# Kernel optimization log

Hardware: AMD Instinct MI355X
Metric: run time of the kernel (lower is better)

The kernel has to match this reference:

```python
import jax, jax.numpy as jnp
import numpy as np

NUM_HEADS = 8
ROPE_BASE = 10000.0

def rotate_half(x):
    x1, x2 = jnp.split(x, 2, axis=-1)
    return jnp.concatenate((-x2, x1), axis=-1)

def rope_cos_sin(seq_len, head_dim, dtype):
    inv_freq = 1.0 / (ROPE_BASE ** (jnp.arange(0, head_dim, 2, dtype=jnp.float32) / head_dim))
    t = jnp.arange(seq_len, dtype=jnp.float32)
    freqs = t[:, None] * inv_freq[None, :]            # [N, D/2]
    emb = jnp.concatenate((freqs, freqs), axis=-1)    # [N, D]
    cos = jnp.cos(emb)[None, None].astype(dtype)      # [1,1,N,D]
    sin = jnp.sin(emb)[None, None].astype(dtype)
    return cos, sin

def setup_inputs() -> dict:
    key = jax.random.key(0)
    k1, k2, k3 = jax.random.split(key, 3)
    B, N, C = 4, 2048, 512
    x = jax.random.normal(k1, (B, N, C), dtype=jnp.float32)
    w_qkv = jax.random.normal(k2, (C, 3 * C), dtype=jnp.float32) * (C ** -0.5)
    w_proj = jax.random.normal(k3, (C, C), dtype=jnp.float32) * (C ** -0.5)
    b_proj = jnp.zeros((C,), dtype=jnp.float32)
    return {"x": x, "w_qkv": w_qkv, "w_proj": w_proj, "b_proj": b_proj}

def reference(x, w_qkv, w_proj, b_proj):
    B, N, C = x.shape
    H = NUM_HEADS
    D = C // H
    scale = D ** -0.5
    qkv = (x @ w_qkv).reshape(B, N, 3, H, D).transpose(2, 0, 3, 1, 4)  # [3,B,H,N,D]
    q, k, v = qkv[0], qkv[1], qkv[2]
    cos, sin = rope_cos_sin(N, D, x.dtype)
    q = q * cos + rotate_half(q) * sin
    k = k * cos + rotate_half(k) * sin
    attn = jax.nn.softmax(jnp.einsum('bhnd,bhmd->bhnm', q, k) * scale, axis=-1)  # [B,H,N,N]
    out = jnp.einsum('bhnm,bhmd->bhnd', attn, v)      # [B,H,N,D]
    out = out.transpose(0, 2, 1, 3).reshape(B, N, C)
    out = out @ w_proj + b_proj
    return out, attn
```

## Files before the change

kernel.cpp:

```cpp
#include <hip/hip_runtime.h>
#include <math.h>


#define OFF_K 4194304
#define OFF_V 8388608

typedef float nf4 __attribute__((ext_vector_type(4)));

#define SWZ(row, col) (((((col) >> 2) ^ (((row) >> 2) & 7)) << 2) | ((col) & 3))

__global__ __launch_bounds__(256) void gemm_qkv_kernel(
    const float* __restrict__ x, const float* __restrict__ w,
    float* __restrict__ qb, float* __restrict__ kb, float* __restrict__ vb)
{
    __shared__ float As[8][132];
    __shared__ float Bs[8][132];
    const int tid  = threadIdx.x;
    const int row0 = blockIdx.x * 128;
    const int col0 = blockIdx.y * 128;
    const int tx = tid & 15, ty = tid >> 4;

    float acc[8][8];
    #pragma unroll
    for (int i = 0; i < 8; ++i)
        #pragma unroll
        for (int j = 0; j < 8; ++j) acc[i][j] = 0.0f;

    const int ar  = tid >> 1;
    const int ah  = (tid & 1) * 4;
    const int bkr = tid >> 5;
    const int bc  = (tid & 31) * 4;

    for (int k0 = 0; k0 < 512; k0 += 8) {
        float4 a4 = *(const float4*)(x + (size_t)(row0 + ar) * 512 + k0 + ah);
        float4 b4 = *(const float4*)(w + (size_t)(k0 + bkr) * 1536 + col0 + bc);
        __syncthreads();
        As[ah + 0][ar] = a4.x; As[ah + 1][ar] = a4.y;
        As[ah + 2][ar] = a4.z; As[ah + 3][ar] = a4.w;
        *(float4*)&Bs[bkr][bc] = b4;
        __syncthreads();
        #pragma unroll
        for (int kk = 0; kk < 8; ++kk) {
            float a[8], b[8];
            *(float4*)&a[0] = *(const float4*)&As[kk][ty * 8];
            *(float4*)&a[4] = *(const float4*)&As[kk][ty * 8 + 4];
            *(float4*)&b[0] = *(const float4*)&Bs[kk][tx * 8];
            *(float4*)&b[4] = *(const float4*)&Bs[kk][tx * 8 + 4];
            #pragma unroll
            for (int i = 0; i < 8; ++i)
                #pragma unroll
                for (int j = 0; j < 8; ++j)
                    acc[i][j] = fmaf(a[i], b[j], acc[i][j]);
        }
    }

    #pragma unroll
    for (int i = 0; i < 8; ++i) {
        int r  = row0 + ty * 8 + i;
        int b_ = r >> 11;
        int n  = r & 2047;
        #pragma unroll
        for (int j0 = 0; j0 < 8; j0 += 4) {
            int c     = col0 + tx * 8 + j0;
            int which = c >> 9;
            int h     = (c >> 6) & 7;
            int d     = c & 63;
            float* base = (which == 0) ? qb : ((which == 1) ? kb : vb);
            float* dst  = base + (((size_t)(b_ * 8 + h) * 2048 + n) * 64 + d);
            *(float4*)dst = make_float4(acc[i][j0], acc[i][j0 + 1],
                                        acc[i][j0 + 2], acc[i][j0 + 3]);
        }
    }
}

__global__ void rope_table_kernel(float2* __restrict__ tab)
{
    int idx = blockIdx.x * 256 + threadIdx.x;
    if (idx >= 2048 * 32) return;
    int i = idx & 31;
    int n = idx >> 5;
    double invf = pow(10000.0, -(double)(2 * i) / 64.0);
    double ang  = (double)n * invf;
    tab[idx] = make_float2((float)cos(ang), (float)sin(ang));
}

__global__ void rope_apply_kernel(float* __restrict__ qb, float* __restrict__ kb,
                                  const float2* __restrict__ tab)
{
    int idx = blockIdx.x * 256 + threadIdx.x;
    if (idx >= 4 * 8 * 2048 * 32) return;
    int i  = idx & 31;
    int n  = (idx >> 5) & 2047;
    int bh = idx >> 16;

    float2 cs = tab[(n << 5) | i];
    float c = cs.x, s = cs.y;

    size_t base = ((size_t)bh * 2048 + n) * 64;
    float q0 = qb[base + i], q1 = qb[base + i + 32];
    qb[base + i]      = q0 * c - q1 * s;
    qb[base + i + 32] = q1 * c + q0 * s;
    float k0 = kb[base + i], k1 = kb[base + i + 32];
    kb[base + i]      = k0 * c - k1 * s;
    kb[base + i + 32] = k1 * c + k0 * s;
}

__global__ __launch_bounds__(256) void attn_scores_pv_kernel(
    const float* __restrict__ qb, const float* __restrict__ kb,
    const float* __restrict__ vb, float* __restrict__ attn,
    float* __restrict__ out_pre)
{
    __shared__ float smem[18560];
    float (*Qs)[128] = (float (*)[128])smem;
    float (*Ks)[128] = (float (*)[128])(smem + 8192);
    float (*Ps)[128] = (float (*)[128])smem;
    float (*Vs)[68]  = (float (*)[68])(smem + 8192);
    float (*mt)[16]  = (float (*)[16])(smem + 16384);
    float* l_lds     = smem + 18432;

    const int tid = threadIdx.x;
    const int bh  = blockIdx.x;
    const int n0  = blockIdx.y * 128;
    const int tx = tid & 15, ty = tid >> 4;

    const float* qbase = qb + ((size_t)bh * 2048 + n0) * 64;
    const float* kbase = kb + (size_t)bh * 2048 * 64;
    const float* vbase = vb + (size_t)bh * 2048 * 64;
    float* attn_base = attn + ((size_t)bh * 2048 + n0) * 2048;

    #pragma unroll
    for (int it = 0; it < 8; ++it) {
        int r = ty + it * 16;
        int d = tx * 4;
        float4 v4 = *(const float4*)(qbase + (size_t)r * 64 + d);
        int pc = SWZ(d, r);
        Qs[d + 0][pc] = v4.x * 0.125f; Qs[d + 1][pc] = v4.y * 0.125f;
        Qs[d + 2][pc] = v4.z * 0.125f; Qs[d + 3][pc] = v4.w * 0.125f;
    }
    float m[8], l[8];
    #pragma unroll
    for (int i = 0; i < 8; ++i) { m[i] = -3.0e38f; l[i] = 0.0f; }
    __syncthreads();

    for (int m0 = 0; m0 < 2048; m0 += 128) {
        float4 kv[8];
        #pragma unroll
        for (int it = 0; it < 8; ++it) {
            int c = ty + it * 16;
            kv[it] = *(const float4*)(kbase + (size_t)(m0 + c) * 64 + tx * 4);
        }
        __syncthreads();
        #pragma unroll
        for (int it = 0; it < 8; ++it) {
            int c = ty + it * 16;
            int d = tx * 4;
            int pc = SWZ(d, c);
            Ks[d + 0][pc] = kv[it].x; Ks[d + 1][pc] = kv[it].y;
            Ks[d + 2][pc] = kv[it].z; Ks[d + 3][pc] = kv[it].w;
        }
        __syncthreads();

        float acc[8][8];
        #pragma unroll
        for (int i = 0; i < 8; ++i)
            #pragma unroll
            for (int j = 0; j < 8; ++j) acc[i][j] = 0.0f;

        #pragma unroll 4
        for (int d = 0; d < 64; ++d) {
            const int sk = (d >> 2) & 7;
            float a[8], b[8];
            *(float4*)&a[0] = *(const float4*)&Qs[d][((ty * 2 + 0) ^ sk) << 2];
            *(float4*)&a[4] = *(const float4*)&Qs[d][((ty * 2 + 1) ^ sk) << 2];
            *(float4*)&b[0] = *(const float4*)&Ks[d][((tx * 2 + 0) ^ sk) << 2];
            *(float4*)&b[4] = *(const float4*)&Ks[d][((tx * 2 + 1) ^ sk) << 2];
            #pragma unroll
            for (int i = 0; i < 8; ++i)
                #pragma unroll
                for (int j = 0; j < 8; ++j)
                    acc[i][j] = fmaf(a[i], b[j], acc[i][j]);
        }

        #pragma unroll
        for (int i = 0; i < 8; ++i) {
            float mx = acc[i][0];
            #pragma unroll
            for (int j = 1; j < 8; ++j) mx = fmaxf(mx, acc[i][j]);
            mx = fmaxf(mx, __shfl_xor(mx, 1));
            mx = fmaxf(mx, __shfl_xor(mx, 2));
            mx = fmaxf(mx, __shfl_xor(mx, 4));
            mx = fmaxf(mx, __shfl_xor(mx, 8));
            float mn = fmaxf(m[i], mx);
            l[i] *= __expf(m[i] - mn);
            m[i]  = mn;
            float s = 0.0f;
            #pragma unroll
            for (int j = 0; j < 8; ++j) {
                acc[i][j] = __expf(acc[i][j] - mn);
                s += acc[i][j];
            }
            s += __shfl_xor(s, 1);
            s += __shfl_xor(s, 2);
            s += __shfl_xor(s, 4);
            s += __shfl_xor(s, 8);
            l[i] += s;
        }

        #pragma unroll
        for (int i = 0; i < 8; ++i) {
            int r = ty * 8 + i;
            float* drow = attn_base + (size_t)r * 2048 + m0 + tx * 8;
            *(float4*)drow       = make_float4(acc[i][0], acc[i][1], acc[i][2], acc[i][3]);
            *(float4*)(drow + 4) = make_float4(acc[i][4], acc[i][5], acc[i][6], acc[i][7]);
        }
        if (tx == 0) {
            int t = m0 >> 7;
            #pragma unroll
            for (int i = 0; i < 8; ++i) mt[ty * 8 + i][t] = m[i];
        }
    }
    if (tx == 0) {
        #pragma unroll
        for (int i = 0; i < 8; ++i) l_lds[ty * 8 + i] = l[i];
    }
    __syncthreads();

    {
        int r  = tid >> 1;
        int c0 = (tid & 1) * 8;
        float v[8];
        #pragma unroll
        for (int j = 0; j < 8; ++j) v[j] = mt[r][c0 + j];
        float mf = mt[r][15];
        float lv = l_lds[r];
        __syncthreads();
        #pragma unroll
        for (int j = 0; j < 8; ++j) mt[r][c0 + j] = __expf(v[j] - mf) / lv;
    }
    __syncthreads();

    float accO[8][4];
    #pragma unroll
    for (int i = 0; i < 8; ++i)
        #pragma unroll
        for (int j = 0; j < 4; ++j) accO[i][j] = 0.0f;

    for (int s0 = 0; s0 < 2048; s0 += 64) {
        const int t = s0 >> 7;
        float4 vv[4];
        #pragma unroll
        for (int it = 0; it < 4; ++it)
            vv[it] = *(const float4*)(vbase + (size_t)(s0 + ty + it * 16) * 64 + tx * 4);

        float4 pp[8];
        #pragma unroll
        for (int it = 0; it < 8; ++it) {
            int r = ty + it * 16;
            float c = mt[r][t];
            float* prow = attn_base + (size_t)r * 2048 + s0 + tx * 4;
            float4 s4 = *(const float4*)prow;
            s4.x *= c; s4.y *= c; s4.z *= c; s4.w *= c;
            pp[it] = s4;
            nf4 nt = { s4.x, s4.y, s4.z, s4.w };
            __builtin_nontemporal_store(nt, (nf4*)prow);
        }

        __syncthreads();
        #pragma unroll
        for (int it = 0; it < 4; ++it)
            *(float4*)&Vs[ty + it * 16][tx * 4] = vv[it];
        #pragma unroll
        for (int it = 0; it < 8; ++it) {
            int r = ty + it * 16;
            int mcol = tx * 4;
            int pc = SWZ(mcol, r);
            Ps[mcol + 0][pc] = pp[it].x; Ps[mcol + 1][pc] = pp[it].y;
            Ps[mcol + 2][pc] = pp[it].z; Ps[mcol + 3][pc] = pp[it].w;
        }
        __syncthreads();

        #pragma unroll 4
        for (int kk = 0; kk < 64; ++kk) {
            const int sk = (kk >> 2) & 7;
            float a[8], b[4];
            *(float4*)&a[0] = *(const float4*)&Ps[kk][((ty * 2 + 0) ^ sk) << 2];
            *(float4*)&a[4] = *(const float4*)&Ps[kk][((ty * 2 + 1) ^ sk) << 2];
            *(float4*)&b[0] = *(const float4*)&Vs[kk][tx * 4];
            #pragma unroll
            for (int i = 0; i < 8; ++i)
                #pragma unroll
                for (int j = 0; j < 4; ++j)
                    accO[i][j] = fmaf(a[i], b[j], accO[i][j]);
        }
    }

    #pragma unroll
    for (int i = 0; i < 8; ++i) {
        float* dst = out_pre + ((size_t)bh * 2048 + n0 + ty * 8 + i) * 64 + tx * 4;
        *(float4*)dst = make_float4(accO[i][0], accO[i][1], accO[i][2], accO[i][3]);
    }
}

__global__ __launch_bounds__(256) void proj_kernel(
    const float* __restrict__ a, const float* __restrict__ w,
    const float* __restrict__ bias, float* __restrict__ out)
{
    __shared__ float As[8][68];
    __shared__ float Bs[8][132];
    const int tid  = threadIdx.x;
    const int row0 = blockIdx.x * 64;
    const int col0 = blockIdx.y * 128;
    const int tx = tid & 31, ty = tid >> 5;

    float acc[8][4];
    #pragma unroll
    for (int i = 0; i < 8; ++i)
        #pragma unroll
        for (int j = 0; j < 4; ++j) acc[i][j] = 0.0f;

    const int ar  = tid >> 1;
    const int ah  = (tid & 1) * 4;
    const int bkr = tid >> 5;
    const int bc  = (tid & 31) * 4;

    const int r_  = row0 + ar;
    const int b_  = r_ >> 11;
    const int n_  = r_ & 2047;

    for (int k0 = 0; k0 < 512; k0 += 8) {
        float4 a4;
        if (tid < 128) {
            const int kk_ = k0 + ah;
            const int h_  = kk_ >> 6;
            const int d_  = kk_ & 63;
            a4 = *(const float4*)(a + (((size_t)(b_ * 8 + h_) * 2048 + n_) * 64 + d_));
        }
        float4 b4 = *(const float4*)(w + (size_t)(k0 + bkr) * 512 + col0 + bc);
        __syncthreads();
        if (tid < 128) {
            As[ah + 0][ar] = a4.x; As[ah + 1][ar] = a4.y;
            As[ah + 2][ar] = a4.z; As[ah + 3][ar] = a4.w;
        }
        *(float4*)&Bs[bkr][bc] = b4;
        __syncthreads();
        #pragma unroll
        for (int kk = 0; kk < 8; ++kk) {
            float av[8], bv[4];
            *(float4*)&av[0] = *(const float4*)&As[kk][ty * 8];
            *(float4*)&av[4] = *(const float4*)&As[kk][ty * 8 + 4];
            *(float4*)&bv[0] = *(const float4*)&Bs[kk][tx * 4];
            #pragma unroll
            for (int i = 0; i < 8; ++i)
                #pragma unroll
                for (int j = 0; j < 4; ++j)
                    acc[i][j] = fmaf(av[i], bv[j], acc[i][j]);
        }
    }

    float bj[4];
    #pragma unroll
    for (int j = 0; j < 4; ++j) bj[j] = bias[col0 + tx * 4 + j];

    #pragma unroll
    for (int i = 0; i < 8; ++i) {
        int r = row0 + ty * 8 + i;
        float* dst = out + (size_t)r * 512 + col0 + tx * 4;
        *(float4*)dst = make_float4(acc[i][0] + bj[0], acc[i][1] + bj[1],
                                    acc[i][2] + bj[2], acc[i][3] + bj[3]);
    }
}

extern "C" void kernel_launch(void* const* d_in, const int* in_sizes, int n_in,
                              void* d_out, int out_size, void* d_ws, size_t ws_size,
                              hipStream_t stream)
{
    const float* x      = (const float*)d_in[0];
    const float* w_qkv  = (const float*)d_in[1];
    const float* w_proj = (const float*)d_in[2];
    const float* b_proj = (const float*)d_in[3];

    float* out  = (float*)d_out;
    float* attn = (float*)d_out + 4194304;

    float* ws = (float*)d_ws;
    float* q = ws;
    float* k = ws + OFF_K;
    float* v = ws + OFF_V;
    float* out_pre = ws;

    float2* rope_tab = (float2*)attn;

    gemm_qkv_kernel<<<dim3(64, 12), 256, 0, stream>>>(x, w_qkv, q, k, v);
    rope_table_kernel<<<256, 256, 0, stream>>>(rope_tab);
    rope_apply_kernel<<<8192, 256, 0, stream>>>(q, k, rope_tab);
    attn_scores_pv_kernel<<<dim3(32, 16), 256, 0, stream>>>(q, k, v, attn, out_pre);
    proj_kernel<<<dim3(128, 4), 256, 0, stream>>>(out_pre, w_proj, b_proj, out);
}
```

Measured before the change: 1.312 ms.

## Fuse RoPE table into apply kernel, pad attention LDS, enlarge proj tiles

Merges the RoPE table generation and application into a single kernel that computes cos/sin once per (n,i) and loops over all batch-head pairs, removing a launch and the table round trip. Pads the attention kernel's shared-memory row stride from 128 to 132 to reduce bank conflicts. Retiles the output projection GEMM to 128x128 blocks with an 8x8 per-thread tile for more register reuse. Risks include lower parallelism in the RoPE kernel, higher register pressure in proj, and the padding interacting with the existing swizzle.

```diff
diff --git a/kernel.cpp b/kernel.cpp
--- a/kernel.cpp
+++ b/kernel.cpp
@@ -73,36 +73,30 @@
     }
 }
 
-__global__ void rope_table_kernel(float2* __restrict__ tab)
+__global__ __launch_bounds__(256) void rope_kernel(
+    float* __restrict__ qb, float* __restrict__ kb)
 {
     int idx = blockIdx.x * 256 + threadIdx.x;
     if (idx >= 2048 * 32) return;
     int i = idx & 31;
     int n = idx >> 5;
+
     double invf = pow(10000.0, -(double)(2 * i) / 64.0);
     double ang  = (double)n * invf;
-    tab[idx] = make_float2((float)cos(ang), (float)sin(ang));
-}
-
-__global__ void rope_apply_kernel(float* __restrict__ qb, float* __restrict__ kb,
-                                  const float2* __restrict__ tab)
-{
-    int idx = blockIdx.x * 256 + threadIdx.x;
-    if (idx >= 4 * 8 * 2048 * 32) return;
-    int i  = idx & 31;
-    int n  = (idx >> 5) & 2047;
-    int bh = idx >> 16;
-
-    float2 cs = tab[(n << 5) | i];
-    float c = cs.x, s = cs.y;
-
-    size_t base = ((size_t)bh * 2048 + n) * 64;
-    float q0 = qb[base + i], q1 = qb[base + i + 32];
-    qb[base + i]      = q0 * c - q1 * s;
-    qb[base + i + 32] = q1 * c + q0 * s;
-    float k0 = kb[base + i], k1 = kb[base + i + 32];
-    kb[base + i]      = k0 * c - k1 * s;
-    kb[base + i + 32] = k1 * c + k0 * s;
+    float c = (float)cos(ang);
+    float s = (float)sin(ang);
+
+    size_t off = (size_t)n * 64 + i;
+    #pragma unroll 4
+    for (int bh = 0; bh < 32; ++bh) {
+        size_t base = (size_t)bh * (2048 * 64) + off;
+        float q0 = qb[base], q1 = qb[base + 32];
+        qb[base]      = q0 * c - q1 * s;
+        qb[base + 32] = q1 * c + q0 * s;
+        float k0 = kb[base], k1 = kb[base + 32];
+        kb[base]      = k0 * c - k1 * s;
+        kb[base + 32] = k1 * c + k0 * s;
+    }
 }
 
 __global__ __launch_bounds__(256) void attn_scores_pv_kernel(
@@ -110,13 +104,13 @@
     const float* __restrict__ vb, float* __restrict__ attn,
     float* __restrict__ out_pre)
 {
-    __shared__ float smem[18560];
-    float (*Qs)[128] = (float (*)[128])smem;
-    float (*Ks)[128] = (float (*)[128])(smem + 8192);
-    float (*Ps)[128] = (float (*)[128])smem;
-    float (*Vs)[68]  = (float (*)[68])(smem + 8192);
-    float (*mt)[16]  = (float (*)[16])(smem + 16384);
-    float* l_lds     = smem + 18432;
+    __shared__ float smem[19072];
+    float (*Qs)[132] = (float (*)[132])smem;
+    float (*Ks)[132] = (float (*)[132])(smem + 8448);
+    float (*Ps)[132] = (float (*)[132])smem;
+    float (*Vs)[68]  = (float (*)[68])(smem + 8448);
+    float (*mt)[16]  = (float (*)[16])(smem + 16896);
+    float* l_lds     = smem + 18944;
 
     const int tid = threadIdx.x;
     const int bh  = blockIdx.x;
@@ -305,18 +299,18 @@
     const float* __restrict__ a, const float* __restrict__ w,
     const float* __restrict__ bias, float* __restrict__ out)
 {
-    __shared__ float As[8][68];
+    __shared__ float As[8][132];
     __shared__ float Bs[8][132];
     const int tid  = threadIdx.x;
-    const int row0 = blockIdx.x * 64;
+    const int row0 = blockIdx.x * 128;
     const int col0 = blockIdx.y * 128;
-    const int tx = tid & 31, ty = tid >> 5;
-
-    float acc[8][4];
+    const int tx = tid & 15, ty = tid >> 4;
+
+    float acc[8][8];
     #pragma unroll
     for (int i = 0; i < 8; ++i)
         #pragma unroll
-        for (int j = 0; j < 4; ++j) acc[i][j] = 0.0f;
+        for (int j = 0; j < 8; ++j) acc[i][j] = 0.0f;
 
     const int ar  = tid >> 1;
     const int ah  = (tid & 1) * 4;
@@ -328,45 +322,43 @@
     const int n_  = r_ & 2047;
 
     for (int k0 = 0; k0 < 512; k0 += 8) {
-        float4 a4;
-        if (tid < 128) {
-            const int kk_ = k0 + ah;
-            const int h_  = kk_ >> 6;
-            const int d_  = kk_ & 63;
-            a4 = *(const float4*)(a + (((size_t)(b_ * 8 + h_) * 2048 + n_) * 64 + d_));
-        }
+        const int kk_ = k0 + ah;
+        const int h_  = kk_ >> 6;
+        const int d_  = kk_ & 63;
+        float4 a4 = *(const float4*)(a + (((size_t)(b_ * 8 + h_) * 2048 + n_) * 64 + d_));
         float4 b4 = *(const float4*)(w + (size_t)(k0 + bkr) * 512 + col0 + bc);
         __syncthreads();
-        if (tid < 128) {
-            As[ah + 0][ar] = a4.x; As[ah + 1][ar] = a4.y;
-            As[ah + 2][ar] = a4.z; As[ah + 3][ar] = a4.w;
-        }
+        As[ah + 0][ar] = a4.x; As[ah + 1][ar] = a4.y;
+        As[ah + 2][ar] = a4.z; As[ah + 3][ar] = a4.w;
         *(float4*)&Bs[bkr][bc] = b4;
         __syncthreads();
         #pragma unroll
         for (int kk = 0; kk < 8; ++kk) {
-            float av[8], bv[4];
+            float av[8], bv[8];
             *(float4*)&av[0] = *(const float4*)&As[kk][ty * 8];
             *(float4*)&av[4] = *(const float4*)&As[kk][ty * 8 + 4];
-            *(float4*)&bv[0] = *(const float4*)&Bs[kk][tx * 4];
+            *(float4*)&bv[0] = *(const float4*)&Bs[kk][tx * 8];
+            *(float4*)&bv[4] = *(const float4*)&Bs[kk][tx * 8 + 4];
             #pragma unroll
             for (int i = 0; i < 8; ++i)
                 #pragma unroll
-                for (int j = 0; j < 4; ++j)
+                for (int j = 0; j < 8; ++j)
                     acc[i][j] = fmaf(av[i], bv[j], acc[i][j]);
         }
     }
 
-    float bj[4];
-    #pragma unroll
-    for (int j = 0; j < 4; ++j) bj[j] = bias[col0 + tx * 4 + j];
+    float bj[8];
+    #pragma unroll
+    for (int j = 0; j < 8; ++j) bj[j] = bias[col0 + tx * 8 + j];
 
     #pragma unroll
     for (int i = 0; i < 8; ++i) {
         int r = row0 + ty * 8 + i;
-        float* dst = out + (size_t)r * 512 + col0 + tx * 4;
-        *(float4*)dst = make_float4(acc[i][0] + bj[0], acc[i][1] + bj[1],
-                                    acc[i][2] + bj[2], acc[i][3] + bj[3]);
+        float* dst = out + (size_t)r * 512 + col0 + tx * 8;
+        *(float4*)dst       = make_float4(acc[i][0] + bj[0], acc[i][1] + bj[1],
+                                          acc[i][2] + bj[2], acc[i][3] + bj[3]);
+        *(float4*)(dst + 4) = make_float4(acc[i][4] + bj[4], acc[i][5] + bj[5],
+                                          acc[i][6] + bj[6], acc[i][7] + bj[7]);
     }
 }
 
@@ -388,11 +380,8 @@
     float* v = ws + OFF_V;
     float* out_pre = ws;
 
-    float2* rope_tab = (float2*)attn;
-
     gemm_qkv_kernel<<<dim3(64, 12), 256, 0, stream>>>(x, w_qkv, q, k, v);
-    rope_table_kernel<<<256, 256, 0, stream>>>(rope_tab);
-    rope_apply_kernel<<<8192, 256, 0, stream>>>(q, k, rope_tab);
+    rope_kernel<<<256, 256, 0, stream>>>(q, k);
     attn_scores_pv_kernel<<<dim3(32, 16), 256, 0, stream>>>(q, k, v, attn, out_pre);
-    proj_kernel<<<dim3(128, 4), 256, 0, stream>>>(out_pre, w_proj, b_proj, out);
-}
+    proj_kernel<<<dim3(64, 4), 256, 0, stream>>>(out_pre, w_proj, b_proj, out);
+}
```

Result: slower. 1.342 ms (+2.3%).
